# Kernel tuning notes

Measured on AMD Instinct MI355X. Metric: run time of the kernel, lower is better.

Reference implementation:

```python
import jax, jax.numpy as jnp
import numpy as np

NEG_INF = -1e9


def setup_inputs() -> dict:
    key = jax.random.key(0)
    ks = jax.random.split(key, 6)
    B, R, D = 32, 4096, 1024
    return {
        "vector": jax.random.normal(ks[0], (B, D), dtype=jnp.float32),
        "matrix": jax.random.normal(ks[1], (B, R, D), dtype=jnp.float32),
        "matrix_mask": jax.random.randint(ks[2], (B, R), 0, 2, dtype=jnp.int32),
        "w_matrix": jax.random.normal(ks[3], (D, D), dtype=jnp.float32) * (1.0 / np.sqrt(D)),
        "u_matrix": jax.random.normal(ks[4], (D, D), dtype=jnp.float32) * (1.0 / np.sqrt(D)),
        "v_vector": jax.random.normal(ks[5], (D, 1), dtype=jnp.float32) * (1.0 / np.sqrt(D)),
    }


def reference(vector, matrix, matrix_mask, w_matrix, u_matrix, v_vector):
    # additive (Bahdanau) scores: tanh(vW + MU) @ v  -> (B, R)
    proj_v = vector @ w_matrix                      # (B, D)
    proj_m = jnp.einsum("brd,de->bre", matrix, u_matrix)  # (B, R, D)
    inter = jnp.tanh(proj_v[:, None, :] + proj_m)   # (B, R, D)
    scores = jnp.einsum("brd,d->br", inter, v_vector[:, 0])  # (B, R)
    # masked softmax over rows
    logits = jnp.where(matrix_mask > 0, scores, NEG_INF)
    return jax.nn.softmax(logits, axis=-1)
```

## Files before the change

kernel.cpp:

```cpp
#include <hip/hip_runtime.h>
#include <cstdint>
#include <cstddef>

#define NEG_INF_F (-1e9f)
static constexpr int Bb = 32;
static constexpr int Rr = 4096;
static constexpr int Dd = 1024;

typedef __attribute__((ext_vector_type(8))) short short8;
typedef __attribute__((ext_vector_type(4))) float floatx4;

__device__ __forceinline__ unsigned short f2bf(float f) {
  unsigned int u = __float_as_uint(f);
  u += 0x7fffu + ((u >> 16) & 1u);
  return (unsigned short)(u >> 16);
}

__global__ void k_uswz(const float* __restrict__ U, unsigned short* __restrict__ Usw) {
  int o = blockIdx.x * 256 + threadIdx.x;
  int j = o & 7;
  int l = (o >> 3) & 63;
  int nt = (o >> 9) & 63;
  int ks = o >> 15;
  int k = ks * 32 + (l >> 4) * 8 + j;
  int n = nt * 16 + (l & 15);
  Usw[o] = f2bf(U[(size_t)k * Dd + n]);
}

__global__ void k_pv(const float* __restrict__ vec, const float* __restrict__ W,
                     float* __restrict__ pv) {
  int e = blockIdx.x * 64 + threadIdx.x;
  int b = blockIdx.y;
  const float* vb = vec + (size_t)b * Dd;
  float acc = 0.f;
#pragma unroll 8
  for (int d = 0; d < Dd; ++d) {
    acc = fmaf(vb[d], W[(size_t)d * Dd + e], acc);
  }
  pv[(size_t)b * Dd + e] = acc;
}

__global__ __launch_bounds__(512, 2)
void k_main(const float* __restrict__ matrix, const unsigned short* __restrict__ Usw,
            const float* __restrict__ pv, const float* __restrict__ vvec,
            float* __restrict__ scores) {
  __shared__ unsigned short As[16384];
  __shared__ float red[512];

  const int t = threadIdx.x;
  const int w = t >> 6;
  const int l = t & 63;
  const int b = blockIdx.y;
  const int r0 = blockIdx.x * 64;
  const float* Ab = matrix + ((size_t)b * Rr + r0) * Dd;

  floatx4 acc[4][8];
#pragma unroll
  for (int mt = 0; mt < 4; ++mt)
#pragma unroll
    for (int nt = 0; nt < 8; ++nt) {
      floatx4 z = {0.f, 0.f, 0.f, 0.f};
      acc[mt][nt] = z;
    }

  const short8* Bs8 = (const short8*)Usw;
  const short8* Aw = ((const short8*)As) + l;

  for (int c = 0; c < 4; ++c) {
    __syncthreads();
#pragma unroll
    for (int i = 0; i < 8; ++i) {
      int idx = i * 512 + t;
      int m = idx >> 6;
      int k4 = idx & 63;
      const float4* src = reinterpret_cast<const float4*>(Ab + (size_t)m * Dd + c * 256);
      float4 f = src[k4];
      int k0 = k4 * 4;
      int ks = k0 >> 5;
      int kin = k0 & 31;
      int quad = kin >> 3;
      int j0 = kin & 7;
      int mt = m >> 4;
      int m16 = m & 15;
      int base = (((ks * 4 + mt) * 64) + quad * 16 + m16) * 8 + j0;
      ushort4 pk;
      pk.x = f2bf(f.x); pk.y = f2bf(f.y); pk.z = f2bf(f.z); pk.w = f2bf(f.w);
      *reinterpret_cast<ushort4*>(&As[base]) = pk;
    }
    __syncthreads();
#pragma unroll
    for (int ks = 0; ks < 8; ++ks) {
      const int ksg = c * 8 + ks;
      short8 a0 = Aw[(ks * 4 + 0) * 64];
      short8 a1 = Aw[(ks * 4 + 1) * 64];
      short8 a2 = Aw[(ks * 4 + 2) * 64];
      short8 a3 = Aw[(ks * 4 + 3) * 64];
      const short8* Bw = Bs8 + ((size_t)ksg * 64 + (size_t)w * 8) * 64 + l;
#pragma unroll
      for (int nt = 0; nt < 8; ++nt) {
        short8 bf = Bw[nt * 64];
        acc[0][nt] = __builtin_amdgcn_mfma_f32_16x16x32_bf16(a0, bf, acc[0][nt], 0, 0, 0);
        acc[1][nt] = __builtin_amdgcn_mfma_f32_16x16x32_bf16(a1, bf, acc[1][nt], 0, 0, 0);
        acc[2][nt] = __builtin_amdgcn_mfma_f32_16x16x32_bf16(a2, bf, acc[2][nt], 0, 0, 0);
        acc[3][nt] = __builtin_amdgcn_mfma_f32_16x16x32_bf16(a3, bf, acc[3][nt], 0, 0, 0);
      }
    }
  }

  float part[4][4];
#pragma unroll
  for (int mt = 0; mt < 4; ++mt)
#pragma unroll
    for (int r = 0; r < 4; ++r) part[mt][r] = 0.f;

  const int n16 = l & 15;
  const int q = l >> 4;
#pragma unroll
  for (int nt = 0; nt < 8; ++nt) {
    const int col = w * 128 + nt * 16 + n16;
    const float pvv = pv[(size_t)b * Dd + col];
    const float vv = vvec[col];
#pragma unroll
    for (int mt = 0; mt < 4; ++mt) {
#pragma unroll
      for (int r = 0; r < 4; ++r) {
        float x = acc[mt][nt][r] + pvv;
        x = fminf(fmaxf(x, -10.f), 10.f);
        float e = __expf(2.f * x);
        float th = (e - 1.f) * __builtin_amdgcn_rcpf(e + 1.f);
        part[mt][r] = fmaf(th, vv, part[mt][r]);
      }
    }
  }
#pragma unroll
  for (int off = 1; off < 16; off <<= 1) {
#pragma unroll
    for (int mt = 0; mt < 4; ++mt)
#pragma unroll
      for (int r = 0; r < 4; ++r)
        part[mt][r] += __shfl_xor(part[mt][r], off, 16);
  }
  if (n16 == 0) {
#pragma unroll
    for (int mt = 0; mt < 4; ++mt)
#pragma unroll
      for (int r = 0; r < 4; ++r) {
        int row = mt * 16 + q * 4 + r;
        red[w * 64 + row] = part[mt][r];
      }
  }
  __syncthreads();
  if (t < 64) {
    float s = 0.f;
#pragma unroll
    for (int ww = 0; ww < 8; ++ww) s += red[ww * 64 + t];
    scores[(size_t)b * Rr + r0 + t] = s;
  }
}

__global__ void k_softmax(const float* __restrict__ scores, const int* __restrict__ mask,
                          float* __restrict__ out) {
  const int b = blockIdx.x;
  const int t = threadIdx.x;
  const float* s = scores + (size_t)b * Rr;
  const int* mk = mask + (size_t)b * Rr;
  float* o = out + (size_t)b * Rr;

  float lg[16];
  float lmax = -3.0e38f;
#pragma unroll
  for (int i = 0; i < 16; ++i) {
    int r = i * 256 + t;
    float x = (mk[r] > 0) ? s[r] : NEG_INF_F;
    lg[i] = x;
    lmax = fmaxf(lmax, x);
  }
#pragma unroll
  for (int off = 1; off < 64; off <<= 1) lmax = fmaxf(lmax, __shfl_xor(lmax, off, 64));
  __shared__ float wb1[4];
  if ((t & 63) == 0) wb1[t >> 6] = lmax;
  __syncthreads();
  lmax = fmaxf(fmaxf(wb1[0], wb1[1]), fmaxf(wb1[2], wb1[3]));

  float lsum = 0.f;
#pragma unroll
  for (int i = 0; i < 16; ++i) {
    float e = __expf(lg[i] - lmax);
    lg[i] = e;
    lsum += e;
  }
#pragma unroll
  for (int off = 1; off < 64; off <<= 1) lsum += __shfl_xor(lsum, off, 64);
  __shared__ float wb2[4];
  if ((t & 63) == 0) wb2[t >> 6] = lsum;
  __syncthreads();
  lsum = wb2[0] + wb2[1] + wb2[2] + wb2[3];
  float inv = 1.0f / lsum;
#pragma unroll
  for (int i = 0; i < 16; ++i) o[i * 256 + t] = lg[i] * inv;
}

extern "C" void kernel_launch(void* const* d_in, const int* in_sizes, int n_in,
                              void* d_out, int out_size, void* d_ws, size_t ws_size,
                              hipStream_t stream) {
  (void)in_sizes; (void)n_in; (void)out_size; (void)ws_size;
  const float* vec = (const float*)d_in[0];
  const float* matrix = (const float*)d_in[1];
  const int* mask = (const int*)d_in[2];
  const float* W = (const float*)d_in[3];
  const float* U = (const float*)d_in[4];
  const float* v = (const float*)d_in[5];
  float* out = (float*)d_out;

  char* ws = (char*)d_ws;
  float* scores = (float*)ws;
  float* pv = (float*)(ws + 524288);
  unsigned short* Usw = (unsigned short*)(ws + 655360);

  k_uswz<<<dim3((Dd * Dd) / 256), dim3(256), 0, stream>>>(U, Usw);
  k_pv<<<dim3(Dd / 64, Bb), dim3(64), 0, stream>>>(vec, W, pv);
  k_main<<<dim3(Rr / 64, Bb), dim3(512), 0, stream>>>(matrix, Usw, pv, v, scores);
  k_softmax<<<dim3(Bb), dim3(256), 0, stream>>>(scores, mask, out);
}
```

Baseline: 1.136 ms.

## Double-buffer A tile via direct global-to-LDS loads and split k_pv reduction

The main GEMM kernel now streams raw fp32 A tiles straight into LDS with global_load_lds into two buffers, so the next K-chunk loads while the current one feeds the MFMAs. The bf16 conversion moves from the staging store to the point where LDS is read. This removes the register round-trip and the extra barrier per chunk, at the cost of twice the LDS bytes per element and conversion work repeated per wave. Separately, k_pv splits its K loop across four waves and reduces through shared memory to raise parallelism.

```diff
diff --git a/kernel.cpp b/kernel.cpp
--- a/kernel.cpp
+++ b/kernel.cpp
@@ -14,6 +14,13 @@
   unsigned int u = __float_as_uint(f);
   u += 0x7fffu + ((u >> 16) & 1u);
   return (unsigned short)(u >> 16);
+}
+
+__device__ __forceinline__ void gload_lds16(const float* g, float* lds) {
+  __builtin_amdgcn_global_load_lds(
+      (const __attribute__((address_space(1))) void*)g,
+      (__attribute__((address_space(3))) void*)lds,
+      16, 0, 0);
 }
 
 __global__ void k_uswz(const float* __restrict__ U, unsigned short* __restrict__ Usw) {
@@ -29,22 +36,28 @@
 
 __global__ void k_pv(const float* __restrict__ vec, const float* __restrict__ W,
                      float* __restrict__ pv) {
-  int e = blockIdx.x * 64 + threadIdx.x;
-  int b = blockIdx.y;
+  __shared__ float r4[4][64];
+  const int l = threadIdx.x & 63;
+  const int kp = threadIdx.x >> 6;
+  const int e = blockIdx.x * 64 + l;
+  const int b = blockIdx.y;
   const float* vb = vec + (size_t)b * Dd;
   float acc = 0.f;
+  const int d0 = kp * 256;
 #pragma unroll 8
-  for (int d = 0; d < Dd; ++d) {
+  for (int d = d0; d < d0 + 256; ++d)
     acc = fmaf(vb[d], W[(size_t)d * Dd + e], acc);
-  }
-  pv[(size_t)b * Dd + e] = acc;
+  r4[kp][l] = acc;
+  __syncthreads();
+  if (kp == 0)
+    pv[(size_t)b * Dd + e] = (r4[0][l] + r4[1][l]) + (r4[2][l] + r4[3][l]);
 }
 
 __global__ __launch_bounds__(512, 2)
 void k_main(const float* __restrict__ matrix, const unsigned short* __restrict__ Usw,
             const float* __restrict__ pv, const float* __restrict__ vvec,
             float* __restrict__ scores) {
-  __shared__ unsigned short As[16384];
+  __shared__ float As[2][4096];
   __shared__ float red[512];
 
   const int t = threadIdx.x;
@@ -54,6 +67,10 @@
   const int r0 = blockIdx.x * 64;
   const float* Ab = matrix + ((size_t)b * Rr + r0) * Dd;
 
+  const int prow = (w & 3) * 16 + (l & 15);
+  const int pk = ((w >> 2) << 5) + ((l >> 4) << 3);
+  const float* gA = Ab + (size_t)prow * Dd + pk;
+
   floatx4 acc[4][8];
 #pragma unroll
   for (int mt = 0; mt < 4; ++mt)
@@ -64,45 +81,44 @@
     }
 
   const short8* Bs8 = (const short8*)Usw;
-  const short8* Aw = ((const short8*)As) + l;
-
-  for (int c = 0; c < 4; ++c) {
+
+  {
+    float* lb = &As[0][(w * 2) << 8];
+    gload_lds16(gA, lb);
+    gload_lds16(gA + 4, lb + 256);
+  }
+
+  for (int c = 0; c < 16; ++c) {
+    const int buf = c & 1;
     __syncthreads();
-#pragma unroll
-    for (int i = 0; i < 8; ++i) {
-      int idx = i * 512 + t;
-      int m = idx >> 6;
-      int k4 = idx & 63;
-      const float4* src = reinterpret_cast<const float4*>(Ab + (size_t)m * Dd + c * 256);
-      float4 f = src[k4];
-      int k0 = k4 * 4;
-      int ks = k0 >> 5;
-      int kin = k0 & 31;
-      int quad = kin >> 3;
-      int j0 = kin & 7;
-      int mt = m >> 4;
-      int m16 = m & 15;
-      int base = (((ks * 4 + mt) * 64) + quad * 16 + m16) * 8 + j0;
-      ushort4 pk;
-      pk.x = f2bf(f.x); pk.y = f2bf(f.y); pk.z = f2bf(f.z); pk.w = f2bf(f.w);
-      *reinterpret_cast<ushort4*>(&As[base]) = pk;
-    }
-    __syncthreads();
-#pragma unroll
-    for (int ks = 0; ks < 8; ++ks) {
-      const int ksg = c * 8 + ks;
-      short8 a0 = Aw[(ks * 4 + 0) * 64];
-      short8 a1 = Aw[(ks * 4 + 1) * 64];
-      short8 a2 = Aw[(ks * 4 + 2) * 64];
-      short8 a3 = Aw[(ks * 4 + 3) * 64];
+    if (c + 1 < 16) {
+      float* lb = &As[buf ^ 1][(w * 2) << 8];
+      const float* g = gA + (c + 1) * 64;
+      gload_lds16(g, lb);
+      gload_lds16(g + 4, lb + 256);
+    }
+#pragma unroll
+    for (int ks2 = 0; ks2 < 2; ++ks2) {
+      const int ksg = c * 2 + ks2;
+      short8 af[4];
+#pragma unroll
+      for (int mt = 0; mt < 4; ++mt) {
+        const float* p0 = &As[buf][(((ks2 * 4 + mt) << 1) << 8) + (l << 2)];
+        float4 lo = *(const float4*)p0;
+        float4 hi = *(const float4*)(p0 + 256);
+        af[mt][0] = (short)f2bf(lo.x); af[mt][1] = (short)f2bf(lo.y);
+        af[mt][2] = (short)f2bf(lo.z); af[mt][3] = (short)f2bf(lo.w);
+        af[mt][4] = (short)f2bf(hi.x); af[mt][5] = (short)f2bf(hi.y);
+        af[mt][6] = (short)f2bf(hi.z); af[mt][7] = (short)f2bf(hi.w);
+      }
       const short8* Bw = Bs8 + ((size_t)ksg * 64 + (size_t)w * 8) * 64 + l;
 #pragma unroll
       for (int nt = 0; nt < 8; ++nt) {
         short8 bf = Bw[nt * 64];
-        acc[0][nt] = __builtin_amdgcn_mfma_f32_16x16x32_bf16(a0, bf, acc[0][nt], 0, 0, 0);
-        acc[1][nt] = __builtin_amdgcn_mfma_f32_16x16x32_bf16(a1, bf, acc[1][nt], 0, 0, 0);
-        acc[2][nt] = __builtin_amdgcn_mfma_f32_16x16x32_bf16(a2, bf, acc[2][nt], 0, 0, 0);
-        acc[3][nt] = __builtin_amdgcn_mfma_f32_16x16x32_bf16(a3, bf, acc[3][nt], 0, 0, 0);
+        acc[0][nt] = __builtin_amdgcn_mfma_f32_16x16x32_bf16(af[0], bf, acc[0][nt], 0, 0, 0);
+        acc[1][nt] = __builtin_amdgcn_mfma_f32_16x16x32_bf16(af[1], bf, acc[1][nt], 0, 0, 0);
+        acc[2][nt] = __builtin_amdgcn_mfma_f32_16x16x32_bf16(af[2], bf, acc[2][nt], 0, 0, 0);
+        acc[3][nt] = __builtin_amdgcn_mfma_f32_16x16x32_bf16(af[3], bf, acc[3][nt], 0, 0, 0);
       }
     }
   }
@@ -218,7 +234,7 @@
   unsigned short* Usw = (unsigned short*)(ws + 655360);
 
   k_uswz<<<dim3((Dd * Dd) / 256), dim3(256), 0, stream>>>(U, Usw);
-  k_pv<<<dim3(Dd / 64, Bb), dim3(64), 0, stream>>>(vec, W, pv);
+  k_pv<<<dim3(Dd / 64, Bb), dim3(256), 0, stream>>>(vec, W, pv);
   k_main<<<dim3(Rr / 64, Bb), dim3(512), 0, stream>>>(matrix, Usw, pv, v, scores);
   k_softmax<<<dim3(Bb), dim3(256), 0, stream>>>(scores, mask, out);
 }
```

Result: faster. 1.032 ms (-9.2%).
